# Optimization experiments

Measured on AMD Instinct MI355X. Metric: run time of the kernel, lower is better.

## Reference

```python
import jax, jax.numpy as jnp
import numpy as np
import math

D = 1024      # d_model
H = 16        # n_heads
DH = 64       # d_head
V = 32000     # vocab_size
MAXS = 2048   # max_seq_length
B, S = 2, 2048
PAD = 0
NEG = -1000000000.0
EPS = 1e-5


def _layernorm(x, g, b):
    mu = jnp.mean(x, axis=-1, keepdims=True)
    var = jnp.mean(jnp.square(x - mu), axis=-1, keepdims=True)
    return (x - mu) * jax.lax.rsqrt(var + EPS) * g + b


def _pad_mask(ids):
    # (b,1,1,S) additive mask over key columns where token == PAD
    return jnp.where((ids == PAD)[:, None, None, :], NEG, 0.0).astype(jnp.float32)


def _attn(Q, K, V_, out_w, out_b, causal_mask, pad_mask):
    # Q,K,V_: [b,n,s,d]
    logits = jnp.einsum('bnqd,bnkd->bnqk', Q, K) / math.sqrt(DH)
    if causal_mask is not None:
        logits = logits + causal_mask
    if pad_mask is not None:
        logits = logits + pad_mask
    probs = jax.nn.softmax(logits, axis=-1)
    o = jnp.einsum('bnqk,bnkd->bnqd', probs, V_)
    b, n, s, d = o.shape
    o = o.transpose(0, 2, 1, 3).reshape(b, s, n * d)  # b s (n d)
    return o @ out_w + out_b


def _heads(x, w, b):
    y = x @ w + b  # [b,s,H*DH]
    bs, s, _ = y.shape
    return y.reshape(bs, s, H, DH).transpose(0, 2, 1, 3)  # b n s d


def setup_inputs() -> dict:
    key = jax.random.key(0)
    ks = jax.random.split(key, 32)
    p = lambda i, shp, sc=0.02: (jax.random.normal(ks[i], shp, jnp.float32) * sc)
    inp = {
        'input_embedding': jax.random.normal(ks[0], (B, S, D), jnp.float32),
        'input_ids': jax.random.randint(ks[1], (B, S), 0, V),
        'target_ids': jax.random.randint(ks[2], (B, S), 0, V),
        'tok_emb': p(3, (V, D), 1.0),
        'pos_emb': p(4, (MAXS, D), 1.0),
        'ln1_g': jnp.ones((D,)), 'ln1_b': jnp.zeros((D,)),
        'q1_w': p(5, (D, H * DH)), 'q1_b': jnp.zeros((H * DH,)),
        'k1_w': p(6, (D, H * DH)), 'k1_b': jnp.zeros((H * DH,)),
        'v1_w': p(7, (D, H * DH)), 'v1_b': jnp.zeros((H * DH,)),
        'out1_w': p(8, (H * DH, D)), 'out1_b': jnp.zeros((D,)),
        'ln2_g': jnp.ones((D,)), 'ln2_b': jnp.zeros((D,)),
        'q2_w': p(9, (D, H * DH)), 'q2_b': jnp.zeros((H * DH,)),
        'k2_w': p(10, (D, H * DH)), 'k2_b': jnp.zeros((H * DH,)),
        'v2_w': p(11, (D, H * DH)), 'v2_b': jnp.zeros((H * DH,)),
        'out2_w': p(12, (H * DH, D)), 'out2_b': jnp.zeros((D,)),
        'ln3_g': jnp.ones((D,)), 'ln3_b': jnp.zeros((D,)),
        'mlp_w1': p(13, (D, 4 * D)), 'mlp_b1': jnp.zeros((4 * D,)),
        'mlp_w2': p(14, (4 * D, D)), 'mlp_b2': jnp.zeros((D,)),
    }
    return inp


def reference(input_embedding, input_ids, target_ids, tok_emb, pos_emb,
              ln1_g, ln1_b, q1_w, q1_b, k1_w, k1_b, v1_w, v1_b, out1_w, out1_b,
              ln2_g, ln2_b, q2_w, q2_b, k2_w, k2_b, v2_w, v2_b, out2_w, out2_b,
              ln3_g, ln3_b, mlp_w1, mlp_b1, mlp_w2, mlp_b2):
    b, s = target_ids.shape
    # embedding + positional
    x = tok_emb[target_ids] + pos_emb[jnp.arange(s)][None, :, :]
    x = _layernorm(x, ln1_g, ln1_b)
    # masked self-attention
    Q = _heads(x, q1_w, q1_b)
    K = _heads(x, k1_w, k1_b)
    Vv = _heads(x, v1_w, v1_b)
    causal = jnp.triu(jnp.full((s, s), NEG, jnp.float32), k=1)[None, None]
    attn = _attn(Q, K, Vv, out1_w, out1_b, causal, _pad_mask(target_ids))
    h = x + attn
    h = _layernorm(h, ln2_g, ln2_b)
    # cross-attention against encoder states
    Qc = _heads(h, q2_w, q2_b)
    Kc = _heads(input_embedding, k2_w, k2_b)
    Vc = _heads(input_embedding, v2_w, v2_b)
    cross = _attn(Qc, Kc, Vc, out2_w, out2_b, None, _pad_mask(input_ids))
    r = cross + h
    # MLP with exact GELU (torch nn.GELU default)
    z = _layernorm(r, ln3_g, ln3_b)
    mlp = jax.nn.gelu(z @ mlp_w1 + mlp_b1, approximate=False) @ mlp_w2 + mlp_b2
    return mlp + r
```

## Files before the change

### kernel.cpp

```cpp
#include <hip/hip_runtime.h>
#include <hip/hip_bf16.h>

#define S_LEN 2048
#define NEGF -1000000000.0f
#define QSC 0.18033688f

typedef unsigned short ushort_t;
typedef __attribute__((ext_vector_type(8))) short short8;
typedef __attribute__((ext_vector_type(4))) float f32x4;

#if defined(__has_builtin)
#if __has_builtin(__builtin_amdgcn_exp2f)
#define EXP2 __builtin_amdgcn_exp2f
#endif
#endif
#ifndef EXP2
#define EXP2 exp2f
#endif

__device__ __forceinline__ unsigned short f2b(float f) {
  unsigned int u = __float_as_uint(f);
  return (unsigned short)((u + 0x7fffu + ((u >> 16) & 1u)) >> 16);
}

__device__ __forceinline__ void gld_lds16(const void* g, void* l) {
  __builtin_amdgcn_global_load_lds((__attribute__((address_space(1))) unsigned int*)g,
                                   (__attribute__((address_space(3))) unsigned int*)l, 16, 0, 0);
}

__device__ __forceinline__ void wtrans_body(const float* __restrict__ W,
                                            ushort_t* __restrict__ Wt, int K, int N,
                                            int bx, int by) {
  __shared__ float t[32][33];
  int n0 = bx * 32, k0 = by * 32;
  int tx = threadIdx.x & 31, ty = threadIdx.x >> 5;
#pragma unroll
  for (int i = 0; i < 32; i += 8)
    t[ty + i][tx] = W[(size_t)(k0 + ty + i) * N + n0 + tx];
  __syncthreads();
#pragma unroll
  for (int i = 0; i < 32; i += 8)
    Wt[(size_t)(n0 + ty + i) * K + k0 + tx] = f2b(t[tx][ty + i]);
}

__global__ __launch_bounds__(256) void wtrans(const float* __restrict__ W,
                                              ushort_t* __restrict__ Wt, int K, int N) {
  wtrans_body(W, Wt, K, N, blockIdx.x, blockIdx.y);
}

struct P8 {
  const float* s[8];
  ushort_t* d[8];
};
__global__ __launch_bounds__(256) void wtrans8(P8 p) {
  wtrans_body(p.s[blockIdx.z], p.d[blockIdx.z], 1024, 1024, blockIdx.x, blockIdx.y);
}

__global__ __launch_bounds__(256) void f2bcvt(const float* __restrict__ in,
                                              ushort_t* __restrict__ out) {
  size_t i = ((size_t)blockIdx.x * 256 + threadIdx.x) * 4;
  float4 v = *(const float4*)(in + i);
  union { unsigned short u[4]; uint2 q; } pk;
  pk.u[0] = f2b(v.x); pk.u[1] = f2b(v.y); pk.u[2] = f2b(v.z); pk.u[3] = f2b(v.w);
  *(uint2*)(out + i) = pk.q;
}

__global__ __launch_bounds__(256) void bcat(float* __restrict__ dst, const float* __restrict__ a,
                                            const float* __restrict__ b,
                                            const float* __restrict__ c, int n0, int n1) {
  int i = blockIdx.x * 256 + threadIdx.x;
  float v = (i < n0) ? a[i] : (i < n0 + n1 ? b[i - n0] : c[i - n0 - n1]);
  dst[i] = v;
}

__device__ __forceinline__ void row_stats(float s, float ss, float* outMean, float* outRstd) {
  __shared__ float red[8];
#pragma unroll
  for (int o = 32; o > 0; o >>= 1) {
    s += __shfl_down(s, o);
    ss += __shfl_down(ss, o);
  }
  int wave = threadIdx.x >> 6, lane = threadIdx.x & 63;
  if (lane == 0) { red[wave] = s; red[4 + wave] = ss; }
  __syncthreads();
  if (threadIdx.x == 0) {
    float S0 = red[0] + red[1] + red[2] + red[3];
    float S1 = red[4] + red[5] + red[6] + red[7];
    float mean = S0 * (1.0f / 1024.0f);
    float var = S1 * (1.0f / 1024.0f) - mean * mean;
    red[0] = mean;
    red[1] = rsqrtf(var + 1e-5f);
  }
  __syncthreads();
  *outMean = red[0];
  *outRstd = red[1];
}

__global__ __launch_bounds__(256) void embed_ln(const int* __restrict__ tids,
                                                const float* __restrict__ tok,
                                                const float* __restrict__ pos,
                                                const float* __restrict__ g,
                                                const float* __restrict__ be,
                                                float* __restrict__ xf,
                                                ushort_t* __restrict__ xb) {
  int row = blockIdx.x;
  int s = row & (S_LEN - 1);
  int id = tids[row];
  int c = threadIdx.x * 4;
  float4 v = *(const float4*)(tok + (size_t)id * 1024 + c);
  float4 p = *(const float4*)(pos + (size_t)s * 1024 + c);
  v.x += p.x; v.y += p.y; v.z += p.z; v.w += p.w;
  float mean, rstd;
  row_stats(v.x + v.y + v.z + v.w, v.x * v.x + v.y * v.y + v.z * v.z + v.w * v.w, &mean, &rstd);
  float4 gv = *(const float4*)(g + c);
  float4 bv = *(const float4*)(be + c);
  float4 o;
  o.x = (v.x - mean) * rstd * gv.x + bv.x;
  o.y = (v.y - mean) * rstd * gv.y + bv.y;
  o.z = (v.z - mean) * rstd * gv.z + bv.z;
  o.w = (v.w - mean) * rstd * gv.w + bv.w;
  *(float4*)(xf + (size_t)row * 1024 + c) = o;
  union { unsigned short u[4]; uint2 q; } pk;
  pk.u[0] = f2b(o.x); pk.u[1] = f2b(o.y); pk.u[2] = f2b(o.z); pk.u[3] = f2b(o.w);
  *(uint2*)(xb + (size_t)row * 1024 + c) = pk.q;
}

__global__ __launch_bounds__(256) void ln_fwd(const float* in, const float* __restrict__ g,
                                              const float* __restrict__ be, float* outF,
                                              ushort_t* __restrict__ outB) {
  int row = blockIdx.x;
  int c = threadIdx.x * 4;
  float4 v = *(const float4*)(in + (size_t)row * 1024 + c);
  float mean, rstd;
  row_stats(v.x + v.y + v.z + v.w, v.x * v.x + v.y * v.y + v.z * v.z + v.w * v.w, &mean, &rstd);
  float4 gv = *(const float4*)(g + c);
  float4 bv = *(const float4*)(be + c);
  float4 o;
  o.x = (v.x - mean) * rstd * gv.x + bv.x;
  o.y = (v.y - mean) * rstd * gv.y + bv.y;
  o.z = (v.z - mean) * rstd * gv.z + bv.z;
  o.w = (v.w - mean) * rstd * gv.w + bv.w;
  if (outF) *(float4*)(outF + (size_t)row * 1024 + c) = o;
  union { unsigned short u[4]; uint2 q; } pk;
  pk.u[0] = f2b(o.x); pk.u[1] = f2b(o.y); pk.u[2] = f2b(o.z); pk.u[3] = f2b(o.w);
  *(uint2*)(outB + (size_t)row * 1024 + c) = pk.q;
}

__global__ __launch_bounds__(256) void gemm_bt(const ushort_t* __restrict__ A,
                                               const ushort_t* __restrict__ Bt,
                                               const float* __restrict__ bias,
                                               const float* __restrict__ res,
                                               float* __restrict__ outF,
                                               ushort_t* __restrict__ outB,
                                               ushort_t* __restrict__ outT,
                                               int M, int N, int K, int act, int scaleN,
                                               int nSplit) {
  __shared__ __align__(16) ushort_t lA[128 * 64];
  __shared__ __align__(16) ushort_t lB[128 * 64];
  const int tid = threadIdx.x;
  const int wave = tid >> 6, lane = tid & 63;
  const int quad = lane >> 4, l16 = lane & 15;
  const int m0 = blockIdx.y * 128, n0 = blockIdx.x * 128;
  const int wm = (wave >> 1) * 64, wn = (wave & 1) * 64;

  f32x4 zero4 = {0.f, 0.f, 0.f, 0.f};
  f32x4 acc[4][4];
#pragma unroll
  for (int i = 0; i < 4; ++i)
#pragma unroll
    for (int j = 0; j < 4; ++j) acc[i][j] = zero4;

  int rowS[4], chkS[4];
#pragma unroll
  for (int ii = 0; ii < 4; ++ii) {
    int d = (wave * 4 + ii) * 64 + lane;
    rowS[ii] = d >> 3;
    chkS[ii] = (d & 7) ^ (rowS[ii] & 7);
  }

  for (int kt = 0; kt < K; kt += 64) {
    __syncthreads();
#pragma unroll
    for (int ii = 0; ii < 4; ++ii) {
      gld_lds16(A + (size_t)(m0 + rowS[ii]) * K + kt + chkS[ii] * 8,
                (char*)lA + (wave * 4 + ii) * 1024);
      gld_lds16(Bt + (size_t)(n0 + rowS[ii]) * K + kt + chkS[ii] * 8,
                (char*)lB + (wave * 4 + ii) * 1024);
    }
    __syncthreads();
#pragma unroll
    for (int kc = 0; kc < 2; ++kc) {
      short8 af[4], bf[4];
#pragma unroll
      for (int mt = 0; mt < 4; ++mt) {
        int r = wm + mt * 16 + l16;
        int c = (kc * 4 + quad) ^ (r & 7);
        af[mt] = *(const short8*)(lA + r * 64 + c * 8);
      }
#pragma unroll
      for (int nt = 0; nt < 4; ++nt) {
        int r = wn + nt * 16 + l16;
        int c = (kc * 4 + quad) ^ (r & 7);
        bf[nt] = *(const short8*)(lB + r * 64 + c * 8);
      }
#pragma unroll
      for (int mt = 0; mt < 4; ++mt)
#pragma unroll
        for (int nt = 0; nt < 4; ++nt)
          acc[mt][nt] = __builtin_amdgcn_mfma_f32_16x16x32_bf16(af[mt], bf[nt], acc[mt][nt], 0, 0, 0);
    }
  }

#pragma unroll
  for (int nt = 0; nt < 4; ++nt) {
    int gn = n0 + wn + nt * 16 + l16;
    float bv = bias[gn];
    if (gn < nSplit) {
#pragma unroll
      for (int mt = 0; mt < 4; ++mt) {
        int gmb = m0 + wm + mt * 16 + quad * 4;
#pragma unroll
        for (int reg = 0; reg < 4; ++reg) {
          size_t idx = (size_t)(gmb + reg) * nSplit + gn;
          float v = acc[mt][nt][reg] + bv;
          if (act == 1) v = 0.5f * v * (1.0f + erff(v * 0.70710678118654752f));
          if (gn < scaleN) v *= QSC;
          if (res) v += res[idx];
          if (outF) outF[idx] = v;
          if (outB) outB[idx] = f2b(v);
        }
      }
    } else {
#pragma unroll
      for (int mt = 0; mt < 4; ++mt) {
        int gmb = m0 + wm + mt * 16 + quad * 4;
        union { unsigned short u[4]; uint2 q; } pk;
#pragma unroll
        for (int reg = 0; reg < 4; ++reg) pk.u[reg] = f2b(acc[mt][nt][reg] + bv);
        *(uint2*)(outT + (size_t)(gn - nSplit) * M + gmb) = pk.q;
      }
    }
  }
}

__global__ __launch_bounds__(512, 2) void gemm256(const ushort_t* __restrict__ A,
                                                  const ushort_t* __restrict__ Bt,
                                                  const float* __restrict__ bias,
                                                  const float* __restrict__ res,
                                                  float* __restrict__ outF,
                                                  ushort_t* __restrict__ outB,
                                                  ushort_t* __restrict__ outT,
                                                  int M, int N, int K, int act, int scaleN,
                                                  int nSplit) {
  __shared__ __align__(16) ushort_t sA[2][256 * 64];
  __shared__ __align__(16) ushort_t sB[2][256 * 64];
  const int tid = threadIdx.x;
  const int wave = tid >> 6, lane = tid & 63;
  const int quad = lane >> 4, l16 = lane & 15;
  const int m0 = blockIdx.y * 256, n0 = blockIdx.x * 256;
  const int wm = (wave >> 2) * 128, wn = (wave & 3) * 64;

  const ushort_t* Ab = A + (size_t)m0 * K;
  const ushort_t* Bb = Bt + (size_t)n0 * K;

  const int srow = tid >> 3;
  const int schk = ((tid & 7) ^ (srow & 7)) << 3;

#define STAGE_H(SRC, LD, KT, DST, H)                                          \
  do {                                                                        \
    gld_lds16((SRC) + (size_t)((H) * 128 + srow) * (LD) + (KT) + schk,        \
              (char*)(DST) + (H) * 16384 + tid * 16);                         \
    gld_lds16((SRC) + (size_t)((H) * 128 + 64 + srow) * (LD) + (KT) + schk,   \
              (char*)(DST) + (H) * 16384 + 8192 + tid * 16);                  \
  } while (0)

  f32x4 zero4 = {0.f, 0.f, 0.f, 0.f};
  f32x4 acc[8][4];
#pragma unroll
  for (int i = 0; i < 8; ++i)
#pragma unroll
    for (int j = 0; j < 4; ++j) acc[i][j] = zero4;

  const int NT = K >> 6;

  STAGE_H(Ab, K, 0, sA[0], 0);
  STAGE_H(Ab, K, 0, sA[0], 1);
  STAGE_H(Bb, K, 0, sB[0], 0);
  STAGE_H(Bb, K, 0, sB[0], 1);
  asm volatile("s_waitcnt vmcnt(0)" ::: "memory");
  __builtin_amdgcn_s_barrier();

  for (int t = 0; t < NT; ++t) {
    const ushort_t* curA = sA[t & 1];
    const ushort_t* curB = sB[t & 1];
    ushort_t* nxtA = sA[(t + 1) & 1];
    ushort_t* nxtB = sB[(t + 1) & 1];
    const int ktn = (t + 1) << 6;
    const bool more = (t + 1 < NT);
#pragma unroll
    for (int q = 0; q < 4; ++q) {
      const int mh = q >> 1, nh = q & 1;
      short8 af[4][2], bf[2][2];
#pragma unroll
      for (int mt = 0; mt < 4; ++mt)
#pragma unroll
        for (int kc = 0; kc < 2; ++kc) {
          int r = wm + (mh * 4 + mt) * 16 + l16;
          af[mt][kc] = *(const short8*)(curA + r * 64 + (((kc * 4 + quad) ^ (r & 7)) << 3));
        }
#pragma unroll
      for (int nt = 0; nt < 2; ++nt)
#pragma unroll
        for (int kc = 0; kc < 2; ++kc) {
          int r = wn + (nh * 2 + nt) * 16 + l16;
          bf[nt][kc] = *(const short8*)(curB + r * 64 + (((kc * 4 + quad) ^ (r & 7)) << 3));
        }
      if (more) {
        if (q == 0) {
          STAGE_H(Ab, K, ktn, nxtA, 0);
          STAGE_H(Ab, K, ktn, nxtA, 1);
        } else if (q == 1) {
          STAGE_H(Bb, K, ktn, nxtB, 0);
          STAGE_H(Bb, K, ktn, nxtB, 1);
        }
      }
      __builtin_amdgcn_s_barrier();
      asm volatile("s_waitcnt lgkmcnt(0)" ::: "memory");
      __builtin_amdgcn_s_setprio(1);
#pragma unroll
      for (int mt = 0; mt < 4; ++mt)
#pragma unroll
        for (int nt = 0; nt < 2; ++nt)
#pragma unroll
          for (int kc = 0; kc < 2; ++kc)
            acc[mh * 4 + mt][nh * 2 + nt] = __builtin_amdgcn_mfma_f32_16x16x32_bf16(
                af[mt][kc], bf[nt][kc], acc[mh * 4 + mt][nh * 2 + nt], 0, 0, 0);
      __builtin_amdgcn_s_setprio(0);
      if (q == 3) asm volatile("s_waitcnt vmcnt(0)" ::: "memory");
      __builtin_amdgcn_s_barrier();
    }
  }
#undef STAGE_H

#pragma unroll
  for (int nt = 0; nt < 4; ++nt) {
    int gn = n0 + wn + nt * 16 + l16;
    float bv = bias[gn];
    if (gn < nSplit) {
#pragma unroll
      for (int mt = 0; mt < 8; ++mt) {
        int gmb = m0 + wm + mt * 16 + quad * 4;
#pragma unroll
        for (int reg = 0; reg < 4; ++reg) {
          size_t idx = (size_t)(gmb + reg) * nSplit + gn;
          float v = acc[mt][nt][reg] + bv;
          if (act == 1) v = 0.5f * v * (1.0f + erff(v * 0.70710678118654752f));
          if (gn < scaleN) v *= QSC;
          if (res) v += res[idx];
          if (outF) outF[idx] = v;
          if (outB) outB[idx] = f2b(v);
        }
      }
    } else {
#pragma unroll
      for (int mt = 0; mt < 8; ++mt) {
        int gmb = m0 + wm + mt * 16 + quad * 4;
        union { unsigned short u[4]; uint2 q2; } pk;
#pragma unroll
        for (int reg = 0; reg < 4; ++reg) pk.u[reg] = f2b(acc[mt][nt][reg] + bv);
        *(uint2*)(outT + (size_t)(gn - nSplit) * M + gmb) = pk.q2;
      }
    }
  }
}

__global__ __launch_bounds__(256) void gemm_n64(const ushort_t* __restrict__ A,
                                                const ushort_t* __restrict__ Bt,
                                                const float* __restrict__ bias,
                                                const float* __restrict__ res,
                                                float* __restrict__ outF,
                                                ushort_t* __restrict__ outB,
                                                int M, int N, int K, int act, int scaleN) {
  __shared__ __align__(16) ushort_t lA[128 * 64];
  __shared__ __align__(16) ushort_t lB[64 * 64];
  const int tid = threadIdx.x;
  const int wave = tid >> 6, lane = tid & 63;
  const int quad = lane >> 4, l16 = lane & 15;
  const int m0 = blockIdx.y * 128, n0 = blockIdx.x * 64;
  const int wm = wave * 32;

  f32x4 zero4 = {0.f, 0.f, 0.f, 0.f};
  f32x4 acc[2][4];
#pragma unroll
  for (int i = 0; i < 2; ++i)
#pragma unroll
    for (int j = 0; j < 4; ++j) acc[i][j] = zero4;

  int rowA[4], chkA[4], rowB[2], chkB[2];
#pragma unroll
  for (int ii = 0; ii < 4; ++ii) {
    int d = (wave * 4 + ii) * 64 + lane;
    rowA[ii] = d >> 3;
    chkA[ii] = (d & 7) ^ (rowA[ii] & 7);
  }
#pragma unroll
  for (int ii = 0; ii < 2; ++ii) {
    int d = (wave * 2 + ii) * 64 + lane;
    rowB[ii] = d >> 3;
    chkB[ii] = (d & 7) ^ (rowB[ii] & 7);
  }

  for (int kt = 0; kt < K; kt += 64) {
    __syncthreads();
#pragma unroll
    for (int ii = 0; ii < 4; ++ii)
      gld_lds16(A + (size_t)(m0 + rowA[ii]) * K + kt + chkA[ii] * 8,
                (char*)lA + (wave * 4 + ii) * 1024);
#pragma unroll
    for (int ii = 0; ii < 2; ++ii)
      gld_lds16(Bt + (size_t)(n0 + rowB[ii]) * K + kt + chkB[ii] * 8,
                (char*)lB + (wave * 2 + ii) * 1024);
    __syncthreads();
#pragma unroll
    for (int kc = 0; kc < 2; ++kc) {
      short8 af[2], bf[4];
#pragma unroll
      for (int mt = 0; mt < 2; ++mt) {
        int r = wm + mt * 16 + l16;
        int c = (kc * 4 + quad) ^ (r & 7);
        af[mt] = *(const short8*)(lA + r * 64 + c * 8);
      }
#pragma unroll
      for (int nt = 0; nt < 4; ++nt) {
        int r = nt * 16 + l16;
        int c = (kc * 4 + quad) ^ (r & 7);
        bf[nt] = *(const short8*)(lB + r * 64 + c * 8);
      }
#pragma unroll
      for (int mt = 0; mt < 2; ++mt)
#pragma unroll
        for (int nt = 0; nt < 4; ++nt)
          acc[mt][nt] = __builtin_amdgcn_mfma_f32_16x16x32_bf16(af[mt], bf[nt], acc[mt][nt], 0, 0, 0);
    }
  }

#pragma unroll
  for (int nt = 0; nt < 4; ++nt) {
    int gn = n0 + nt * 16 + l16;
    float bv = bias[gn];
#pragma unroll
    for (int mt = 0; mt < 2; ++mt) {
      int gmb = m0 + wm + mt * 16 + quad * 4;
#pragma unroll
      for (int reg = 0; reg < 4; ++reg) {
        size_t idx = (size_t)(gmb + reg) * N + gn;
        float v = acc[mt][nt][reg] + bv;
        if (act == 1) v = 0.5f * v * (1.0f + erff(v * 0.70710678118654752f));
        if (gn < scaleN) v *= QSC;
        if (res) v += res[idx];
        if (outF) outF[idx] = v;
        if (outB) outB[idx] = f2b(v);
      }
    }
  }
}

template <int CAUSAL>
__global__ __launch_bounds__(256, 4) void attn3(const ushort_t* __restrict__ Qp, int ldQ,
                                                const ushort_t* __restrict__ Kp, int ldK,
                                                const ushort_t* __restrict__ Vt,
                                                const int* __restrict__ ids,
                                                ushort_t* __restrict__ O) {
  __shared__ float pm[S_LEN];
  __shared__ __align__(16) ushort_t lK[64 * 64];
  __shared__ __align__(16) ushort_t lVt[64 * 64];
  __shared__ __align__(16) ushort_t lP[4][16 * 64];

  const int h = blockIdx.y, b = blockIdx.z;
  const int g = CAUSAL ? (31 - (int)blockIdx.x) : (int)blockIdx.x;
  const int tid = threadIdx.x;
  const int wave = tid >> 6, lane = tid & 63;
  const int quad = lane >> 4, l16 = lane & 15;
  const int g0 = g * 64;

  for (int i = tid; i < S_LEN; i += 256)
    pm[i] = (ids[b * S_LEN + i] == 0) ? NEGF : 0.0f;

  const int qrow = g0 + wave * 16 + l16;
  const ushort_t* qb = Qp + ((size_t)(b * S_LEN) + qrow) * ldQ + h * 64;
  short8 qf[2];
  qf[0] = *(const short8*)(qb + quad * 8);
  qf[1] = *(const short8*)(qb + 32 + quad * 8);

  f32x4 zero4 = {0.f, 0.f, 0.f, 0.f};
  f32x4 acc_o[4];
#pragma unroll
  for (int nt = 0; nt < 4; ++nt) acc_o[nt] = zero4;
  float lsum[4] = {0.f, 0.f, 0.f, 0.f};

  const int nkv = CAUSAL ? (g + 1) : (S_LEN / 64);
  const int qbase = g0 + wave * 16 + quad * 4;

  for (int kv = 0; kv < nkv; ++kv) {
    const int kv0 = kv * 64;
    __syncthreads();
#pragma unroll
    for (int ii = 0; ii < 2; ++ii) {
      int slot = (wave * 2 + ii) * 64 + lane;
      int row = slot >> 3;
      int cs = (slot & 7) ^ (row & 7);
      gld_lds16(Kp + (size_t)(b * S_LEN + kv0 + row) * ldK + h * 64 + cs * 8,
                (char*)lK + (wave * 2 + ii) * 1024);
      gld_lds16(Vt + (size_t)(h * 64 + row) * 4096 + b * S_LEN + kv0 + cs * 8,
                (char*)lVt + (wave * 2 + ii) * 1024);
    }
    __syncthreads();

    f32x4 sacc[4];
#pragma unroll
    for (int nt = 0; nt < 4; ++nt) sacc[nt] = zero4;
#pragma unroll
    for (int kc = 0; kc < 2; ++kc) {
#pragma unroll
      for (int nt = 0; nt < 4; ++nt) {
        int r = nt * 16 + l16;
        int c = (kc * 4 + quad) ^ (r & 7);
        short8 kf = *(const short8*)(lK + r * 64 + c * 8);
        sacc[nt] = __builtin_amdgcn_mfma_f32_16x16x32_bf16(qf[kc], kf, sacc[nt], 0, 0, 0);
      }
    }

    const bool diag = CAUSAL && (kv == g);
#pragma unroll
    for (int nt = 0; nt < 4; ++nt) {
      float pmv = pm[kv0 + nt * 16 + l16];
      int kk = kv0 + nt * 16 + l16;
#pragma unroll
      for (int reg = 0; reg < 4; ++reg) {
        float s = sacc[nt][reg] + pmv;
        if (diag && kk > qbase + reg) s = NEGF;
        float p = EXP2(s);
        lsum[reg] += p;
        int q = quad * 4 + reg;
        int cc = (nt * 2 + (l16 >> 3)) ^ (q & 7);
        lP[wave][q * 64 + cc * 8 + (l16 & 7)] = f2b(p);
      }
    }

#pragma unroll
    for (int kc = 0; kc < 2; ++kc) {
      int cp = (kc * 4 + quad) ^ (l16 & 7);
      short8 pf = *(const short8*)(&lP[wave][l16 * 64 + cp * 8]);
#pragma unroll
      for (int nt = 0; nt < 4; ++nt) {
        int r = nt * 16 + l16;
        int c = (kc * 4 + quad) ^ (r & 7);
        short8 vf = *(const short8*)(lVt + r * 64 + c * 8);
        acc_o[nt] = __builtin_amdgcn_mfma_f32_16x16x32_bf16(pf, vf, acc_o[nt], 0, 0, 0);
      }
    }
  }

  float inv[4];
#pragma unroll
  for (int reg = 0; reg < 4; ++reg) {
    float t = lsum[reg];
    t += __shfl_xor(t, 1);
    t += __shfl_xor(t, 2);
    t += __shfl_xor(t, 4);
    t += __shfl_xor(t, 8);
    inv[reg] = 1.0f / t;
  }
#pragma unroll
  for (int nt = 0; nt < 4; ++nt)
#pragma unroll
    for (int reg = 0; reg < 4; ++reg) {
      int qr = g0 + wave * 16 + quad * 4 + reg;
      O[((size_t)(b * S_LEN) + qr) * 1024 + h * 64 + nt * 16 + l16] =
          f2b(acc_o[nt][reg] * inv[reg]);
    }
}

extern "C" void kernel_launch(void* const* d_in, const int* in_sizes, int n_in,
                              void* d_out, int out_size, void* d_ws, size_t ws_size,
                              hipStream_t stream) {
  (void)in_sizes; (void)n_in; (void)out_size; (void)ws_size;
  const size_t MB = 1024 * 1024;
  char* w = (char*)d_ws;
  ushort_t* qkv1T = (ushort_t*)(w + 0);
  ushort_t* o1T = (ushort_t*)(w + 6 * MB);
  ushort_t* q2T = (ushort_t*)(w + 8 * MB);
  ushort_t* k2v2T = (ushort_t*)(w + 10 * MB);
  ushort_t* o2T = (ushort_t*)(w + 14 * MB);
  ushort_t* m1T = (ushort_t*)(w + 16 * MB);
  ushort_t* m2T = (ushort_t*)(w + 24 * MB);
  float* bias3 = (float*)(w + 32 * MB);
  float* bias2 = (float*)(w + 32 * MB + 64 * 1024);
  ushort_t* xb = (ushort_t*)(w + 33 * MB);
  ushort_t* QKb = (ushort_t*)(w + 41 * MB);
  ushort_t* Vt = (ushort_t*)(w + 57 * MB);
  ushort_t* Ob = (ushort_t*)(w + 65 * MB);
  ushort_t* encb = (ushort_t*)(w + 73 * MB);
  float* xf = (float*)(w + 81 * MB);
  float* hf = (float*)(w + 97 * MB);
  ushort_t* m1b = (ushort_t*)(w + 113 * MB);
  ushort_t* hlnb = xb;
  ushort_t* Q2b = QKb;
  ushort_t* K2b = QKb + 4 * MB;

  dim3 B256(256);
  dim3 B512(512);
  P8 p8;
  p8.s[0] = (const float*)d_in[7];  p8.d[0] = qkv1T;
  p8.s[1] = (const float*)d_in[9];  p8.d[1] = qkv1T + 1024 * 1024;
  p8.s[2] = (const float*)d_in[11]; p8.d[2] = qkv1T + 2 * 1024 * 1024;
  p8.s[3] = (const float*)d_in[13]; p8.d[3] = o1T;
  p8.s[4] = (const float*)d_in[17]; p8.d[4] = q2T;
  p8.s[5] = (const float*)d_in[19]; p8.d[5] = k2v2T;
  p8.s[6] = (const float*)d_in[21]; p8.d[6] = k2v2T + 1024 * 1024;
  p8.s[7] = (const float*)d_in[23]; p8.d[7] = o2T;
  wtrans8<<<dim3(32, 32, 8), B256, 0, stream>>>(p8);
  wtrans<<<dim3(128, 32), B256, 0, stream>>>((const float*)d_in[27], m1T, 1024, 4096);
  wtrans<<<dim3(32, 128), B256, 0, stream>>>((const float*)d_in[29], m2T, 4096, 1024);
  f2bcvt<<<4096, B256, 0, stream>>>((const float*)d_in[0], encb);
  bcat<<<12, B256, 0, stream>>>(bias3, (const float*)d_in[8], (const float*)d_in[10],
                                (const float*)d_in[12], 1024, 1024);
  bcat<<<8, B256, 0, stream>>>(bias2, (const float*)d_in[20], (const float*)d_in[22],
                               (const float*)d_in[22], 1024, 1024);

  embed_ln<<<4096, B256, 0, stream>>>((const int*)d_in[2], (const float*)d_in[3],
                                      (const float*)d_in[4], (const float*)d_in[5],
                                      (const float*)d_in[6], xf, xb);
  gemm256<<<dim3(12, 16), B512, 0, stream>>>(xb, qkv1T, bias3, nullptr, nullptr, QKb, Vt,
                                             4096, 3072, 1024, 0, 1024, 2048);
  attn3<1><<<dim3(32, 16, 2), B256, 0, stream>>>(QKb, 2048, QKb + 1024, 2048, Vt,
                                                 (const int*)d_in[2], Ob);
  gemm_n64<<<dim3(16, 32), B256, 0, stream>>>(Ob, o1T, (const float*)d_in[14], xf, hf, nullptr,
                                              4096, 1024, 1024, 0, 0);
  ln_fwd<<<4096, B256, 0, stream>>>(hf, (const float*)d_in[15], (const float*)d_in[16], hf, hlnb);
  gemm_n64<<<dim3(16, 32), B256, 0, stream>>>(hlnb, q2T, (const float*)d_in[18], nullptr, nullptr,
                                              Q2b, 4096, 1024, 1024, 0, 1024);
  gemm256<<<dim3(8, 16), B512, 0, stream>>>(encb, k2v2T, bias2, nullptr, nullptr, K2b, Vt,
                                            4096, 2048, 1024, 0, 0, 1024);
  attn3<0><<<dim3(32, 16, 2), B256, 0, stream>>>(Q2b, 1024, K2b, 1024, Vt,
                                                 (const int*)d_in[1], Ob);
  gemm_n64<<<dim3(16, 32), B256, 0, stream>>>(Ob, o2T, (const float*)d_in[24], hf, xf, nullptr,
                                              4096, 1024, 1024, 0, 0);
  ln_fwd<<<4096, B256, 0, stream>>>(xf, (const float*)d_in[25], (const float*)d_in[26], nullptr,
                                    hlnb);
  gemm256<<<dim3(16, 16), B512, 0, stream>>>(hlnb, m1T, (const float*)d_in[28], nullptr, nullptr,
                                             m1b, nullptr, 4096, 4096, 1024, 1, 0, 4096);
  gemm_n64<<<dim3(16, 32), B256, 0, stream>>>(m1b, m2T, (const float*)d_in[30], xf, (float*)d_out,
                                              nullptr, 4096, 1024, 4096, 0, 0);
}
```

Before: 748.5 us.

## Double-buffer LDS staging in gemm_n64 and attention, precompute pad masks

Adds a second LDS buffer to the N=64 GEMM and to the attention kernel, so the next K/V or A/B tile is loaded while MFMAs run on the current one. This leaves one barrier per iteration instead of two. Pad masks are now built once by a small kernel and read from global memory, replacing the per-block LDS fill. The QKV and cross K/V projections switch from gemm256 to gemm_bt with a different grid. The extra buffers double LDS use, which may reduce occupancy, especially for the attention kernel.

```diff
diff --git a/kernel.cpp b/kernel.cpp
--- a/kernel.cpp
+++ b/kernel.cpp
@@ -71,6 +71,15 @@
   int i = blockIdx.x * 256 + threadIdx.x;
   float v = (i < n0) ? a[i] : (i < n0 + n1 ? b[i - n0] : c[i - n0 - n1]);
   dst[i] = v;
+}
+
+__global__ __launch_bounds__(256) void padmask(const int* __restrict__ tids,
+                                               const int* __restrict__ iids,
+                                               float* __restrict__ pmA,
+                                               float* __restrict__ pmB) {
+  int i = blockIdx.x * 256 + threadIdx.x;
+  pmA[i] = (tids[i] == 0) ? NEGF : 0.0f;
+  pmB[i] = (iids[i] == 0) ? NEGF : 0.0f;
 }
 
 __device__ __forceinline__ void row_stats(float s, float ss, float* outMean, float* outRstd) {
@@ -381,8 +390,8 @@
                                                 float* __restrict__ outF,
                                                 ushort_t* __restrict__ outB,
                                                 int M, int N, int K, int act, int scaleN) {
-  __shared__ __align__(16) ushort_t lA[128 * 64];
-  __shared__ __align__(16) ushort_t lB[64 * 64];
+  __shared__ __align__(16) ushort_t lA[2][128 * 64];
+  __shared__ __align__(16) ushort_t lB[2][64 * 64];
   const int tid = threadIdx.x;
   const int wave = tid >> 6, lane = tid & 63;
   const int quad = lane >> 4, l16 = lane & 15;
@@ -410,17 +419,24 @@
     chkB[ii] = (d & 7) ^ (rowB[ii] & 7);
   }
 
+#define STG64(KT, BUF)                                                         \
+  do {                                                                         \
+    _Pragma("unroll") for (int ii = 0; ii < 4; ++ii)                           \
+        gld_lds16(A + (size_t)(m0 + rowA[ii]) * K + (KT) + chkA[ii] * 8,       \
+                  (char*)lA[BUF] + (wave * 4 + ii) * 1024);                    \
+    _Pragma("unroll") for (int ii = 0; ii < 2; ++ii)                           \
+        gld_lds16(Bt + (size_t)(n0 + rowB[ii]) * K + (KT) + chkB[ii] * 8,      \
+                  (char*)lB[BUF] + (wave * 2 + ii) * 1024);                    \
+  } while (0)
+
+  STG64(0, 0);
+  __syncthreads();
+
+  int cur = 0;
   for (int kt = 0; kt < K; kt += 64) {
-    __syncthreads();
-#pragma unroll
-    for (int ii = 0; ii < 4; ++ii)
-      gld_lds16(A + (size_t)(m0 + rowA[ii]) * K + kt + chkA[ii] * 8,
-                (char*)lA + (wave * 4 + ii) * 1024);
-#pragma unroll
-    for (int ii = 0; ii < 2; ++ii)
-      gld_lds16(Bt + (size_t)(n0 + rowB[ii]) * K + kt + chkB[ii] * 8,
-                (char*)lB + (wave * 2 + ii) * 1024);
-    __syncthreads();
+    if (kt + 64 < K) STG64(kt + 64, cur ^ 1);
+    const ushort_t* cA = lA[cur];
+    const ushort_t* cB = lB[cur];
 #pragma unroll
     for (int kc = 0; kc < 2; ++kc) {
       short8 af[2], bf[4];
@@ -428,13 +444,13 @@
       for (int mt = 0; mt < 2; ++mt) {
         int r = wm + mt * 16 + l16;
         int c = (kc * 4 + quad) ^ (r & 7);
-        af[mt] = *(const short8*)(lA + r * 64 + c * 8);
+        af[mt] = *(const short8*)(cA + r * 64 + c * 8);
       }
 #pragma unroll
       for (int nt = 0; nt < 4; ++nt) {
         int r = nt * 16 + l16;
         int c = (kc * 4 + quad) ^ (r & 7);
-        bf[nt] = *(const short8*)(lB + r * 64 + c * 8);
+        bf[nt] = *(const short8*)(cB + r * 64 + c * 8);
       }
 #pragma unroll
       for (int mt = 0; mt < 2; ++mt)
@@ -442,7 +458,10 @@
         for (int nt = 0; nt < 4; ++nt)
           acc[mt][nt] = __builtin_amdgcn_mfma_f32_16x16x32_bf16(af[mt], bf[nt], acc[mt][nt], 0, 0, 0);
     }
-  }
+    __syncthreads();
+    cur ^= 1;
+  }
+#undef STG64
 
 #pragma unroll
   for (int nt = 0; nt < 4; ++nt) {
@@ -466,14 +485,13 @@
 }
 
 template <int CAUSAL>
-__global__ __launch_bounds__(256, 4) void attn3(const ushort_t* __restrict__ Qp, int ldQ,
+__global__ __launch_bounds__(256, 4) void attn4(const ushort_t* __restrict__ Qp, int ldQ,
                                                 const ushort_t* __restrict__ Kp, int ldK,
                                                 const ushort_t* __restrict__ Vt,
-                                                const int* __restrict__ ids,
+                                                const float* __restrict__ pmg,
                                                 ushort_t* __restrict__ O) {
-  __shared__ float pm[S_LEN];
-  __shared__ __align__(16) ushort_t lK[64 * 64];
-  __shared__ __align__(16) ushort_t lVt[64 * 64];
+  __shared__ __align__(16) ushort_t lK[2][64 * 64];
+  __shared__ __align__(16) ushort_t lV[2][64 * 64];
   __shared__ __align__(16) ushort_t lP[4][16 * 64];
 
   const int h = blockIdx.y, b = blockIdx.z;
@@ -482,9 +500,7 @@
   const int wave = tid >> 6, lane = tid & 63;
   const int quad = lane >> 4, l16 = lane & 15;
   const int g0 = g * 64;
-
-  for (int i = tid; i < S_LEN; i += 256)
-    pm[i] = (ids[b * S_LEN + i] == 0) ? NEGF : 0.0f;
+  const float* pmb = pmg + b * S_LEN;
 
   const int qrow = g0 + wave * 16 + l16;
   const ushort_t* qb = Qp + ((size_t)(b * S_LEN) + qrow) * ldQ + h * 64;
@@ -501,20 +517,38 @@
   const int nkv = CAUSAL ? (g + 1) : (S_LEN / 64);
   const int qbase = g0 + wave * 16 + quad * 4;
 
+  int srow[2], scs[2];
+#pragma unroll
+  for (int ii = 0; ii < 2; ++ii) {
+    int slot = (wave * 2 + ii) * 64 + lane;
+    srow[ii] = slot >> 3;
+    scs[ii] = ((slot & 7) ^ (srow[ii] & 7)) * 8;
+  }
+
+#define STAGE_KV(KV0, BUF)                                                            \
+  do {                                                                                \
+    _Pragma("unroll") for (int ii = 0; ii < 2; ++ii) {                                \
+      gld_lds16(Kp + (size_t)(b * S_LEN + (KV0) + srow[ii]) * ldK + h * 64 + scs[ii], \
+                (char*)lK[BUF] + (wave * 2 + ii) * 1024);                             \
+      gld_lds16(Vt + (size_t)(h * 64 + srow[ii]) * 4096 + b * S_LEN + (KV0) + scs[ii],\
+                (char*)lV[BUF] + (wave * 2 + ii) * 1024);                             \
+    }                                                                                 \
+  } while (0)
+
+  STAGE_KV(0, 0);
+  __syncthreads();
+
+  int cur = 0;
   for (int kv = 0; kv < nkv; ++kv) {
     const int kv0 = kv * 64;
-    __syncthreads();
-#pragma unroll
-    for (int ii = 0; ii < 2; ++ii) {
-      int slot = (wave * 2 + ii) * 64 + lane;
-      int row = slot >> 3;
-      int cs = (slot & 7) ^ (row & 7);
-      gld_lds16(Kp + (size_t)(b * S_LEN + kv0 + row) * ldK + h * 64 + cs * 8,
-                (char*)lK + (wave * 2 + ii) * 1024);
-      gld_lds16(Vt + (size_t)(h * 64 + row) * 4096 + b * S_LEN + kv0 + cs * 8,
-                (char*)lVt + (wave * 2 + ii) * 1024);
-    }
-    __syncthreads();
+    if (kv + 1 < nkv) STAGE_KV(kv0 + 64, cur ^ 1);
+
+    float pmv[4];
+#pragma unroll
+    for (int nt = 0; nt < 4; ++nt) pmv[nt] = pmb[kv0 + nt * 16 + l16];
+
+    const ushort_t* cK = lK[cur];
+    const ushort_t* cV = lV[cur];
 
     f32x4 sacc[4];
 #pragma unroll
@@ -525,7 +559,7 @@
       for (int nt = 0; nt < 4; ++nt) {
         int r = nt * 16 + l16;
         int c = (kc * 4 + quad) ^ (r & 7);
-        short8 kf = *(const short8*)(lK + r * 64 + c * 8);
+        short8 kf = *(const short8*)(cK + r * 64 + c * 8);
         sacc[nt] = __builtin_amdgcn_mfma_f32_16x16x32_bf16(qf[kc], kf, sacc[nt], 0, 0, 0);
       }
     }
@@ -533,11 +567,10 @@
     const bool diag = CAUSAL && (kv == g);
 #pragma unroll
     for (int nt = 0; nt < 4; ++nt) {
-      float pmv = pm[kv0 + nt * 16 + l16];
       int kk = kv0 + nt * 16 + l16;
 #pragma unroll
       for (int reg = 0; reg < 4; ++reg) {
-        float s = sacc[nt][reg] + pmv;
+        float s = sacc[nt][reg] + pmv[nt];
         if (diag && kk > qbase + reg) s = NEGF;
         float p = EXP2(s);
         lsum[reg] += p;
@@ -555,11 +588,14 @@
       for (int nt = 0; nt < 4; ++nt) {
         int r = nt * 16 + l16;
         int c = (kc * 4 + quad) ^ (r & 7);
-        short8 vf = *(const short8*)(lVt + r * 64 + c * 8);
+        short8 vf = *(const short8*)(cV + r * 64 + c * 8);
         acc_o[nt] = __builtin_amdgcn_mfma_f32_16x16x32_bf16(pf, vf, acc_o[nt], 0, 0, 0);
       }
     }
-  }
+    __syncthreads();
+    cur ^= 1;
+  }
+#undef STAGE_KV
 
   float inv[4];
 #pragma unroll
@@ -596,6 +632,8 @@
   ushort_t* m2T = (ushort_t*)(w + 24 * MB);
   float* bias3 = (float*)(w + 32 * MB);
   float* bias2 = (float*)(w + 32 * MB + 64 * 1024);
+  float* pmA = (float*)(w + 32 * MB + 128 * 1024);
+  float* pmB = (float*)(w + 32 * MB + 160 * 1024);
   ushort_t* xb = (ushort_t*)(w + 33 * MB);
   ushort_t* QKb = (ushort_t*)(w + 41 * MB);
   ushort_t* Vt = (ushort_t*)(w + 57 * MB);
@@ -627,23 +665,22 @@
                                 (const float*)d_in[12], 1024, 1024);
   bcat<<<8, B256, 0, stream>>>(bias2, (const float*)d_in[20], (const float*)d_in[22],
                                (const float*)d_in[22], 1024, 1024);
+  padmask<<<16, B256, 0, stream>>>((const int*)d_in[2], (const int*)d_in[1], pmA, pmB);
 
   embed_ln<<<4096, B256, 0, stream>>>((const int*)d_in[2], (const float*)d_in[3],
                                       (const float*)d_in[4], (const float*)d_in[5],
                                       (const float*)d_in[6], xf, xb);
-  gemm256<<<dim3(12, 16), B512, 0, stream>>>(xb, qkv1T, bias3, nullptr, nullptr, QKb, Vt,
+  gemm_bt<<<dim3(24, 32), B256, 0, stream>>>(xb, qkv1T, bias3, nullptr, nullptr, QKb, Vt,
                                              4096, 3072, 1024, 0, 1024, 2048);
-  attn3<1><<<dim3(32, 16, 2), B256, 0, stream>>>(QKb, 2048, QKb + 1024, 2048, Vt,
-                                                 (const int*)d_in[2], Ob);
+  attn4<1><<<dim3(32, 16, 2), B256, 0, stream>>>(QKb, 2048, QKb + 1024, 2048, Vt, pmA, Ob);
   gemm_n64<<<dim3(16, 32), B256, 0, stream>>>(Ob, o1T, (const float*)d_in[14], xf, hf, nullptr,
                                               4096, 1024, 1024, 0, 0);
   ln_fwd<<<4096, B256, 0, stream>>>(hf, (const float*)d_in[15], (const float*)d_in[16], hf, hlnb);
   gemm_n64<<<dim3(16, 32), B256, 0, stream>>>(hlnb, q2T, (const float*)d_in[18], nullptr, nullptr,
                                               Q2b, 4096, 1024, 1024, 0, 1024);
-  gemm256<<<dim3(8, 16), B512, 0, stream>>>(encb, k2v2T, bias2, nullptr, nullptr, K2b, Vt,
-                                            4096, 2048, 1024, 0, 0, 1024);
-  attn3<0><<<dim3(32, 16, 2), B256, 0, stream>>>(Q2b, 1024, K2b, 1024, Vt,
-                                                 (const int*)d_in[1], Ob);
+  gemm_bt<<<dim3(16, 32), B256, 0, stream>>>(encb, k2v2T, bias2, nullptr, nullptr, K2b, Vt,
+                                             4096, 2048, 1024, 0, 0, 1024);
+  attn4<0><<<dim3(32, 16, 2), B256, 0, stream>>>(Q2b, 1024, K2b, 1024, Vt, pmB, Ob);
   gemm_n64<<<dim3(16, 32), B256, 0, stream>>>(Ob, o2T, (const float*)d_in[24], hf, xf, nullptr,
                                               4096, 1024, 1024, 0, 0);
   ln_fwd<<<4096, B256, 0, stream>>>(xf, (const float*)d_in[25], (const float*)d_in[26], nullptr,
```

After: 710.0 us. 1.05x faster.
